# Optimization experiments

Measured on AMD Instinct MI355X. Metric: run time of the kernel, lower is better.

## Reference

```python
import jax, jax.numpy as jnp
import numpy as np

FILTER_LENGTH = 1024
HOP_LENGTH = 512
CUTOFF = FILTER_LENGTH // 2 + 1  # 513


def _make_forward_basis():
    n = FILTER_LENGTH
    fb = np.fft.fft(np.eye(n))
    fb = np.vstack([np.real(fb[:CUTOFF, :]), np.imag(fb[:CUTOFF, :])]).astype(np.float32)  # [2*cutoff, n]
    # hann window, fftbins=True (periodic); win_length == filter_length so pad_center is a no-op
    win = (0.5 - 0.5 * np.cos(2.0 * np.pi * np.arange(n) / n)).astype(np.float32)
    return jnp.asarray(fb * win[None, :])


def setup_inputs() -> dict:
    key = jax.random.key(0)
    B, T = 8, 1048576
    input_data = jax.random.normal(key, (B, T), dtype=jnp.float32)
    return {
        "input_data": input_data,
        "forward_basis": _make_forward_basis(),  # [1026, 1024]
        "eps": jnp.float32(1e-9),
    }


def reference(input_data, forward_basis, eps):
    pad = FILTER_LENGTH // 2
    x = jnp.pad(input_data, ((0, 0), (pad, pad)), mode="reflect")  # [B, T + filter_length]
    n_frames = (x.shape[1] - FILTER_LENGTH) // HOP_LENGTH + 1
    # gather overlapping frames: [B, n_frames, filter_length]
    idx = jnp.arange(n_frames)[:, None] * HOP_LENGTH + jnp.arange(FILTER_LENGTH)[None, :]
    frames = x[:, idx]
    # DFT via dense matmul: [B, 2*cutoff, n_frames]
    ft = jnp.einsum("fk,bnk->bfn", forward_basis, frames)
    real, imag = ft[:, :CUTOFF, :], ft[:, CUTOFF:, :]
    return jnp.sqrt(real * real + imag * imag + eps)
```

## Files before the change

kernel.cpp:

```cpp
#include <hip/hip_runtime.h>

#define T_LEN   1048576
#define NPAD    1049600
#define NFRAMES 2049
#define BATCH   8
#define NJ      (BATCH * NFRAMES)
#define NSEG    2050
#define CUT     513
#define MROWS   1026
#define MPAD    1152
#define OUT_BF  (CUT * NFRAMES)

typedef __attribute__((ext_vector_type(8))) short bf16x8_t;
typedef __attribute__((ext_vector_type(4))) float f32x4_t;

static __device__ __forceinline__ ushort f2bf(float f) {
    union { float f; unsigned u; } a;
    a.f = f;
    unsigned r = a.u + 0x7fffu + ((a.u >> 16) & 1u);
    return (ushort)(r >> 16);
}

static __device__ __forceinline__ void gl_lds16(const ushort* g, ushort* s) {
    __builtin_amdgcn_global_load_lds(
        (__attribute__((address_space(1))) void*)g,
        (__attribute__((address_space(3))) void*)s,
        16, 0, 0);
}

__global__ void pad_kernel(const float* __restrict__ in, ushort* __restrict__ xpad) {
    int g  = blockIdx.x * 256 + threadIdx.x;
    int b  = g / (NPAD / 8);
    int c  = g - b * (NPAD / 8);
    int i0 = c * 8;
    const float* inb = in + (size_t)b * T_LEN;
    ushort o[8];
    if (i0 >= 512 && i0 + 7 < 512 + T_LEN) {
        const float4 v0 = *(const float4*)(inb + (i0 - 512));
        const float4 v1 = *(const float4*)(inb + (i0 - 512) + 4);
        o[0]=f2bf(v0.x); o[1]=f2bf(v0.y); o[2]=f2bf(v0.z); o[3]=f2bf(v0.w);
        o[4]=f2bf(v1.x); o[5]=f2bf(v1.y); o[6]=f2bf(v1.z); o[7]=f2bf(v1.w);
    } else {
        for (int t = 0; t < 8; ++t) {
            int i = i0 + t;
            int src = (i < 512) ? (512 - i)
                    : (i < 512 + T_LEN) ? (i - 512)
                    : (2 * T_LEN + 510 - i);
            o[t] = f2bf(inb[src]);
        }
    }
    *(ulonglong2*)(xpad + (size_t)b * NPAD + i0) = *(ulonglong2*)o;
}

__global__ void basis_kernel(const float* __restrict__ fb, ushort* __restrict__ A2) {
    int g  = blockIdx.x * 256 + threadIdx.x;
    int r  = g >> 8;
    int cq = (g & 255) * 4;
    ushort4 o;
    if (r < MROWS) {
        int f = r >> 1, h = r & 1;
        const float4 v = *(const float4*)(fb + (size_t)(f + h * CUT) * 1024 + cq);
        o = make_ushort4(f2bf(v.x), f2bf(v.y), f2bf(v.z), f2bf(v.w));
    } else {
        o = make_ushort4(0, 0, 0, 0);
    }
    *(ushort4*)(A2 + (size_t)r * 1024 + cq) = o;
}

__global__ __launch_bounds__(256) void gemm_kernel(
        const ushort* __restrict__ A2, const ushort* __restrict__ xpad,
        float* __restrict__ out, const float* __restrict__ epsp) {
    __shared__ __align__(16) ushort ldsA0[128 * 64];
    __shared__ __align__(16) ushort ldsA1[128 * 64];
    __shared__ __align__(16) ushort ldsB [136 * 64];

    const int tid  = threadIdx.x;
    const int wave = tid >> 6, lane = tid & 63;
    const int quad = lane >> 4, l15 = lane & 15;
    const int m0 = blockIdx.x * 128;
    const int j0 = blockIdx.y * 128;
    const int wm = (wave >> 1) * 64;
    const int wj = (wave & 1) * 64;

    const int sr  = lane >> 3;
    const int sc8 = ((lane & 7) ^ sr) * 8;

    const int b0 = j0 / NFRAMES;
    const int S0 = j0 + b0;

    int aoff[4], boff[4], boffx = 0;
    for (int t = 0; t < 4; ++t) {
        const int r = (wave * 4 + t) * 8 + sr;
        aoff[t] = (m0 + r) * 1024 + sc8;
        int S = S0 + r; if (S > BATCH * NSEG - 1) S = BATCH * NSEG - 1;
        int bb = S / NSEG, ss = S - bb * NSEG;
        boff[t] = bb * NPAD + ss * 512 + sc8;
    }
    {
        int S = S0 + 128 + sr; if (S > BATCH * NSEG - 1) S = BATCH * NSEG - 1;
        int bb = S / NSEG, ss = S - bb * NSEG;
        boffx = bb * NPAD + ss * 512 + sc8;
    }

    int rowb[4];
    for (int jx = 0; jx < 4; ++jx) {
        const int j = j0 + wj + jx * 16 + l15;
        rowb[jx] = wj + jx * 16 + l15 + (j / NFRAMES - b0);
    }

    f32x4_t acc[4][4] = {};

    for (int kt = 0; kt < 8; ++kt) {
        const int k0 = kt * 64;
        __syncthreads();
        for (int t = 0; t < 4; ++t) {
            gl_lds16(A2 + aoff[t] + k0,        &ldsA0[(wave * 4 + t) * 512]);
            gl_lds16(A2 + aoff[t] + 512 + k0,  &ldsA1[(wave * 4 + t) * 512]);
            gl_lds16(xpad + boff[t] + k0,      &ldsB [(wave * 4 + t) * 512]);
        }
        if (wave == 0) gl_lds16(xpad + boffx + k0, &ldsB[16 * 512]);
        __syncthreads();
        for (int kk = 0; kk < 2; ++kk) {
            const int cb = kk * 4 + quad;
            bf16x8_t a0[4], a1[4], bf0[4], bf1[4];
            const int asw = (cb ^ (l15 & 7)) * 8;
            for (int i = 0; i < 4; ++i) {
                const int ro = (wm + i * 16 + l15) * 64;
                a0[i] = *(const bf16x8_t*)&ldsA0[ro + asw];
                a1[i] = *(const bf16x8_t*)&ldsA1[ro + asw];
            }
            for (int jx = 0; jx < 4; ++jx) {
                const int r0 = rowb[jx];
                const int r1 = r0 + 1;
                bf0[jx] = *(const bf16x8_t*)&ldsB[r0 * 64 + ((cb ^ (r0 & 7)) * 8)];
                bf1[jx] = *(const bf16x8_t*)&ldsB[r1 * 64 + ((cb ^ (r1 & 7)) * 8)];
            }
            for (int i = 0; i < 4; ++i)
                for (int jx = 0; jx < 4; ++jx) {
                    acc[i][jx] = __builtin_amdgcn_mfma_f32_16x16x32_bf16(
                        a0[i], bf0[jx], acc[i][jx], 0, 0, 0);
                    acc[i][jx] = __builtin_amdgcn_mfma_f32_16x16x32_bf16(
                        a1[i], bf1[jx], acc[i][jx], 0, 0, 0);
                }
        }
    }

    const float eps = *epsp;
    for (int tj = 0; tj < 4; ++tj) {
        const int j = j0 + wj + tj * 16 + l15;
        if (j >= NJ) continue;
        const int b = j / NFRAMES;
        const int n = j - b * NFRAMES;
        float* ob = out + (size_t)b * OUT_BF + n;
        for (int ti = 0; ti < 4; ++ti) {
            const int M  = m0 + wm + ti * 16 + quad * 4;
            const int f0 = M >> 1;
            f32x4_t a = acc[ti][tj];
            if (f0 < CUT)
                ob[(size_t)f0 * NFRAMES] = sqrtf(a.x * a.x + a.y * a.y + eps);
            if (f0 + 1 < CUT)
                ob[(size_t)(f0 + 1) * NFRAMES] = sqrtf(a.z * a.z + a.w * a.w + eps);
        }
    }
}

extern "C" void kernel_launch(void* const* d_in, const int* in_sizes, int n_in,
                              void* d_out, int out_size, void* d_ws, size_t ws_size,
                              hipStream_t stream) {
    const float* in   = (const float*)d_in[0];
    const float* fb   = (const float*)d_in[1];
    const float* epsp = (const float*)d_in[2];
    float* out = (float*)d_out;

    ushort* A2   = (ushort*)d_ws;
    ushort* xpad = (ushort*)((char*)d_ws + (size_t)MPAD * 1024 * 2);

    pad_kernel<<<dim3(BATCH * (NPAD / 8) / 256), dim3(256), 0, stream>>>(in, xpad);
    basis_kernel<<<dim3(MPAD), dim3(256), 0, stream>>>(fb, A2);
    gemm_kernel<<<dim3(MPAD / 128, (NJ + 127) / 128), dim3(256), 0, stream>>>(A2, xpad, out, epsp);
}
```

Baseline: 134.8 us.

## Halve GEMM k-tile LDS footprint, raise occupancy, and remap blocks for L2 locality

The GEMM k-step drops from 64 to 32 with a new swizzled LDS layout, which halves shared memory per block so more blocks fit per CU. Launch bounds now request 5 blocks per SM. The 2D grid becomes a 1D grid remapped so groups of 8 frame tiles share the 9 basis tiles, aiming at better L2 reuse. LDS read addresses are precomputed into registers. The trade-off is twice as many barrier and load rounds per tile and some idle blocks that exit early.

```diff
diff --git a/kernel.cpp b/kernel.cpp
--- a/kernel.cpp
+++ b/kernel.cpp
@@ -6,10 +6,12 @@
 #define BATCH   8
 #define NJ      (BATCH * NFRAMES)
 #define NSEG    2050
+#define SMAX    (BATCH * NSEG - 1)
 #define CUT     513
 #define MROWS   1026
 #define MPAD    1152
 #define OUT_BF  (CUT * NFRAMES)
+#define NJT     129
 
 typedef __attribute__((ext_vector_type(8))) short bf16x8_t;
 typedef __attribute__((ext_vector_type(4))) float f32x4_t;
@@ -67,82 +69,107 @@
     *(ushort4*)(A2 + (size_t)r * 1024 + cq) = o;
 }
 
-__global__ __launch_bounds__(256) void gemm_kernel(
+__global__ __launch_bounds__(256, 5) void gemm_kernel(
         const ushort* __restrict__ A2, const ushort* __restrict__ xpad,
         float* __restrict__ out, const float* __restrict__ epsp) {
-    __shared__ __align__(16) ushort ldsA0[128 * 64];
-    __shared__ __align__(16) ushort ldsA1[128 * 64];
-    __shared__ __align__(16) ushort ldsB [136 * 64];
+    __shared__ __align__(16) ushort ldsA0[64 * 64];
+    __shared__ __align__(16) ushort ldsA1[64 * 64];
+    __shared__ __align__(16) ushort ldsB [72 * 64];
+
+    const int bid = blockIdx.x;
+    const int jt  = (bid / 72) * 8 + (bid & 7);
+    const int mt  = (bid >> 3) % 9;
+    if (jt >= NJT) return;
 
     const int tid  = threadIdx.x;
     const int wave = tid >> 6, lane = tid & 63;
     const int quad = lane >> 4, l15 = lane & 15;
-    const int m0 = blockIdx.x * 128;
-    const int j0 = blockIdx.y * 128;
+    const int m0 = mt * 128;
+    const int j0 = jt * 128;
     const int wm = (wave >> 1) * 64;
     const int wj = (wave & 1) * 64;
 
-    const int sr  = lane >> 3;
-    const int sc8 = ((lane & 7) ^ sr) * 8;
-
     const int b0 = j0 / NFRAMES;
     const int S0 = j0 + b0;
 
-    int aoff[4], boff[4], boffx = 0;
-    for (int t = 0; t < 4; ++t) {
-        const int r = (wave * 4 + t) * 8 + sr;
-        aoff[t] = (m0 + r) * 1024 + sc8;
-        int S = S0 + r; if (S > BATCH * NSEG - 1) S = BATCH * NSEG - 1;
+    const int li   = lane >> 3;
+    const int lc   = (lane & 7) ^ li;
+    const int half = lc >> 2;
+    const int kch8 = (lc & 3) * 8;
+
+    int aoff[2];
+    for (int t = 0; t < 2; ++t) {
+        const int q = wave * 2 + t;
+        const int arow = (8 * q + li) + 64 * half;
+        aoff[t] = (m0 + arow) * 1024 + kch8;
+    }
+    int boff[2], boffx = 0;
+    for (int t = 0; t < 2; ++t) {
+        const int q = wave * 2 + t;
+        int S = S0 + (8 * q + li) + 72 * half; if (S > SMAX) S = SMAX;
         int bb = S / NSEG, ss = S - bb * NSEG;
-        boff[t] = bb * NPAD + ss * 512 + sc8;
+        boff[t] = bb * NPAD + ss * 512 + kch8;
     }
     {
-        int S = S0 + 128 + sr; if (S > BATCH * NSEG - 1) S = BATCH * NSEG - 1;
+        int S = S0 + (64 + li) + 72 * half; if (S > SMAX) S = SMAX;
         int bb = S / NSEG, ss = S - bb * NSEG;
-        boffx = bb * NPAD + ss * 512 + sc8;
-    }
-
-    int rowb[4];
+        boffx = bb * NPAD + ss * 512 + kch8;
+    }
+
+    int addrA[4], addrB0[4], addrB1[4];
+    for (int i = 0; i < 4; ++i) {
+        const int m  = wm + i * 16 + l15;
+        const int lr = m & 63;
+        const int p  = (((m >> 6) << 2) + quad) ^ (lr & 7);
+        addrA[i] = lr * 64 + p * 8;
+    }
     for (int jx = 0; jx < 4; ++jx) {
-        const int j = j0 + wj + jx * 16 + l15;
-        rowb[jx] = wj + jx * 16 + l15 + (j / NFRAMES - b0);
+        const int j  = j0 + wj + jx * 16 + l15;
+        const int r0 = wj + jx * 16 + l15 + (j / NFRAMES - b0);
+        const int r1 = r0 + 1;
+        const int lr0 = (r0 >= 72) ? r0 - 72 : r0;
+        const int lr1 = (r1 >= 72) ? r1 - 72 : r1;
+        const int p0  = (((r0 >= 72) ? 4 : 0) + quad) ^ (lr0 & 7);
+        const int p1  = (((r1 >= 72) ? 4 : 0) + quad) ^ (lr1 & 7);
+        addrB0[jx] = lr0 * 64 + p0 * 8;
+        addrB1[jx] = lr1 * 64 + p1 * 8;
     }
 
     f32x4_t acc[4][4] = {};
 
-    for (int kt = 0; kt < 8; ++kt) {
-        const int k0 = kt * 64;
+    for (int kt = 0; kt < 16; ++kt) {
+        const int k32 = kt * 32;
         __syncthreads();
-        for (int t = 0; t < 4; ++t) {
-            gl_lds16(A2 + aoff[t] + k0,        &ldsA0[(wave * 4 + t) * 512]);
-            gl_lds16(A2 + aoff[t] + 512 + k0,  &ldsA1[(wave * 4 + t) * 512]);
-            gl_lds16(xpad + boff[t] + k0,      &ldsB [(wave * 4 + t) * 512]);
-        }
-        if (wave == 0) gl_lds16(xpad + boffx + k0, &ldsB[16 * 512]);
+        #pragma unroll
+        for (int t = 0; t < 2; ++t) {
+            const int q = wave * 2 + t;
+            gl_lds16(A2 + aoff[t] + k32,        &ldsA0[q * 512]);
+            gl_lds16(A2 + aoff[t] + 512 + k32,  &ldsA1[q * 512]);
+            gl_lds16(xpad + boff[t] + k32,      &ldsB [q * 512]);
+        }
+        if (wave == 0) gl_lds16(xpad + boffx + k32, &ldsB[8 * 512]);
         __syncthreads();
-        for (int kk = 0; kk < 2; ++kk) {
-            const int cb = kk * 4 + quad;
-            bf16x8_t a0[4], a1[4], bf0[4], bf1[4];
-            const int asw = (cb ^ (l15 & 7)) * 8;
-            for (int i = 0; i < 4; ++i) {
-                const int ro = (wm + i * 16 + l15) * 64;
-                a0[i] = *(const bf16x8_t*)&ldsA0[ro + asw];
-                a1[i] = *(const bf16x8_t*)&ldsA1[ro + asw];
+
+        bf16x8_t a0[4], a1[4], bf0[4], bf1[4];
+        #pragma unroll
+        for (int i = 0; i < 4; ++i) {
+            a0[i] = *(const bf16x8_t*)&ldsA0[addrA[i]];
+            a1[i] = *(const bf16x8_t*)&ldsA1[addrA[i]];
+        }
+        #pragma unroll
+        for (int jx = 0; jx < 4; ++jx) {
+            bf0[jx] = *(const bf16x8_t*)&ldsB[addrB0[jx]];
+            bf1[jx] = *(const bf16x8_t*)&ldsB[addrB1[jx]];
+        }
+        #pragma unroll
+        for (int i = 0; i < 4; ++i)
+            #pragma unroll
+            for (int jx = 0; jx < 4; ++jx) {
+                acc[i][jx] = __builtin_amdgcn_mfma_f32_16x16x32_bf16(
+                    a0[i], bf0[jx], acc[i][jx], 0, 0, 0);
+                acc[i][jx] = __builtin_amdgcn_mfma_f32_16x16x32_bf16(
+                    a1[i], bf1[jx], acc[i][jx], 0, 0, 0);
             }
-            for (int jx = 0; jx < 4; ++jx) {
-                const int r0 = rowb[jx];
-                const int r1 = r0 + 1;
-                bf0[jx] = *(const bf16x8_t*)&ldsB[r0 * 64 + ((cb ^ (r0 & 7)) * 8)];
-                bf1[jx] = *(const bf16x8_t*)&ldsB[r1 * 64 + ((cb ^ (r1 & 7)) * 8)];
-            }
-            for (int i = 0; i < 4; ++i)
-                for (int jx = 0; jx < 4; ++jx) {
-                    acc[i][jx] = __builtin_amdgcn_mfma_f32_16x16x32_bf16(
-                        a0[i], bf0[jx], acc[i][jx], 0, 0, 0);
-                    acc[i][jx] = __builtin_amdgcn_mfma_f32_16x16x32_bf16(
-                        a1[i], bf1[jx], acc[i][jx], 0, 0, 0);
-                }
-        }
     }
 
     const float eps = *epsp;
@@ -177,5 +204,5 @@
 
     pad_kernel<<<dim3(BATCH * (NPAD / 8) / 256), dim3(256), 0, stream>>>(in, xpad);
     basis_kernel<<<dim3(MPAD), dim3(256), 0, stream>>>(fb, A2);
-    gemm_kernel<<<dim3(MPAD / 128, (NJ + 127) / 128), dim3(256), 0, stream>>>(A2, xpad, out, epsp);
-}
+    gemm_kernel<<<dim3(17 * 72), dim3(256), 0, stream>>>(A2, xpad, out, epsp);
+}
```

Result: slower. 146.6 us (+8.8%).

## Double-buffer B tiles in LDS, load A from global, fuse prep kernels, swizzle grid

Applied to the files above, without the earlier changes.

Merges the pad and basis conversion kernels into one launch. In the GEMM, the A (basis) operand is now read directly from global memory into registers instead of staged through LDS, and the B (frames) tile is double-buffered with a prefetch of the next k-slice before computing the current one, removing one barrier per iteration. The grid becomes 1D with a grouped mapping of 8 j-tiles across 9 m-tiles for L2 reuse, and launch_bounds asks for 3 blocks per CU. The risk is that uncoalesced global A loads add latency and register pressure.

```diff
diff --git a/kernel.cpp b/kernel.cpp
--- a/kernel.cpp
+++ b/kernel.cpp
@@ -6,10 +6,13 @@
 #define BATCH   8
 #define NJ      (BATCH * NFRAMES)
 #define NSEG    2050
+#define SMAX    (BATCH * NSEG - 1)
 #define CUT     513
 #define MROWS   1026
 #define MPAD    1152
 #define OUT_BF  (CUT * NFRAMES)
+#define NJT     129
+#define PAD_BLOCKS (BATCH * (NPAD / 8) / 256)
 
 typedef __attribute__((ext_vector_type(8))) short bf16x8_t;
 typedef __attribute__((ext_vector_type(4))) float f32x4_t;
@@ -28,114 +31,132 @@
         16, 0, 0);
 }
 
-__global__ void pad_kernel(const float* __restrict__ in, ushort* __restrict__ xpad) {
-    int g  = blockIdx.x * 256 + threadIdx.x;
-    int b  = g / (NPAD / 8);
-    int c  = g - b * (NPAD / 8);
-    int i0 = c * 8;
-    const float* inb = in + (size_t)b * T_LEN;
-    ushort o[8];
-    if (i0 >= 512 && i0 + 7 < 512 + T_LEN) {
-        const float4 v0 = *(const float4*)(inb + (i0 - 512));
-        const float4 v1 = *(const float4*)(inb + (i0 - 512) + 4);
-        o[0]=f2bf(v0.x); o[1]=f2bf(v0.y); o[2]=f2bf(v0.z); o[3]=f2bf(v0.w);
-        o[4]=f2bf(v1.x); o[5]=f2bf(v1.y); o[6]=f2bf(v1.z); o[7]=f2bf(v1.w);
+__global__ void prep_kernel(const float* __restrict__ in, const float* __restrict__ fb,
+                            ushort* __restrict__ xpad, ushort* __restrict__ A2) {
+    const int tid = threadIdx.x;
+    if (blockIdx.x < PAD_BLOCKS) {
+        int g  = blockIdx.x * 256 + tid;
+        int b  = g / (NPAD / 8);
+        int c  = g - b * (NPAD / 8);
+        int i0 = c * 8;
+        const float* inb = in + (size_t)b * T_LEN;
+        ushort o[8];
+        if (i0 >= 512 && i0 + 7 < 512 + T_LEN) {
+            const float4 v0 = *(const float4*)(inb + (i0 - 512));
+            const float4 v1 = *(const float4*)(inb + (i0 - 512) + 4);
+            o[0]=f2bf(v0.x); o[1]=f2bf(v0.y); o[2]=f2bf(v0.z); o[3]=f2bf(v0.w);
+            o[4]=f2bf(v1.x); o[5]=f2bf(v1.y); o[6]=f2bf(v1.z); o[7]=f2bf(v1.w);
+        } else {
+            for (int t = 0; t < 8; ++t) {
+                int i = i0 + t;
+                int src = (i < 512) ? (512 - i)
+                        : (i < 512 + T_LEN) ? (i - 512)
+                        : (2 * T_LEN + 510 - i);
+                o[t] = f2bf(inb[src]);
+            }
+        }
+        *(ulonglong2*)(xpad + (size_t)b * NPAD + i0) = *(ulonglong2*)o;
     } else {
-        for (int t = 0; t < 8; ++t) {
-            int i = i0 + t;
-            int src = (i < 512) ? (512 - i)
-                    : (i < 512 + T_LEN) ? (i - 512)
-                    : (2 * T_LEN + 510 - i);
-            o[t] = f2bf(inb[src]);
-        }
-    }
-    *(ulonglong2*)(xpad + (size_t)b * NPAD + i0) = *(ulonglong2*)o;
-}
-
-__global__ void basis_kernel(const float* __restrict__ fb, ushort* __restrict__ A2) {
-    int g  = blockIdx.x * 256 + threadIdx.x;
-    int r  = g >> 8;
-    int cq = (g & 255) * 4;
-    ushort4 o;
-    if (r < MROWS) {
-        int f = r >> 1, h = r & 1;
-        const float4 v = *(const float4*)(fb + (size_t)(f + h * CUT) * 1024 + cq);
-        o = make_ushort4(f2bf(v.x), f2bf(v.y), f2bf(v.z), f2bf(v.w));
-    } else {
-        o = make_ushort4(0, 0, 0, 0);
-    }
-    *(ushort4*)(A2 + (size_t)r * 1024 + cq) = o;
-}
-
-__global__ __launch_bounds__(256) void gemm_kernel(
+        int g  = (blockIdx.x - PAD_BLOCKS) * 256 + tid;
+        int r  = g >> 8;
+        int cq = (g & 255) * 4;
+        ushort4 o;
+        if (r < MROWS) {
+            int f = r >> 1, h = r & 1;
+            const float4 v = *(const float4*)(fb + (size_t)(f + h * CUT) * 1024 + cq);
+            o = make_ushort4(f2bf(v.x), f2bf(v.y), f2bf(v.z), f2bf(v.w));
+        } else {
+            o = make_ushort4(0, 0, 0, 0);
+        }
+        *(ushort4*)(A2 + (size_t)r * 1024 + cq) = o;
+    }
+}
+
+__global__ __launch_bounds__(256, 3) void gemm_kernel(
         const ushort* __restrict__ A2, const ushort* __restrict__ xpad,
         float* __restrict__ out, const float* __restrict__ epsp) {
-    __shared__ __align__(16) ushort ldsA0[128 * 64];
-    __shared__ __align__(16) ushort ldsA1[128 * 64];
-    __shared__ __align__(16) ushort ldsB [136 * 64];
+    __shared__ __align__(16) ushort ldsB[2][136 * 64];
+
+    const int bid = blockIdx.x;
+    const int jt  = (bid / 72) * 8 + (bid & 7);
+    const int mt  = (bid >> 3) % 9;
+    if (jt >= NJT) return;
 
     const int tid  = threadIdx.x;
     const int wave = tid >> 6, lane = tid & 63;
     const int quad = lane >> 4, l15 = lane & 15;
-    const int m0 = blockIdx.x * 128;
-    const int j0 = blockIdx.y * 128;
-    const int wm = (wave >> 1) * 64;
-    const int wj = (wave & 1) * 64;
+    const int m0 = mt * 128, j0 = jt * 128;
+    const int wm = (wave >> 1) * 64, wj = (wave & 1) * 64;
+    const int b0 = j0 / NFRAMES;
+    const int S0 = j0 + b0;
 
     const int sr  = lane >> 3;
     const int sc8 = ((lane & 7) ^ sr) * 8;
-
-    const int b0 = j0 / NFRAMES;
-    const int S0 = j0 + b0;
-
-    int aoff[4], boff[4], boffx = 0;
+    int boff[4], boffx;
     for (int t = 0; t < 4; ++t) {
-        const int r = (wave * 4 + t) * 8 + sr;
-        aoff[t] = (m0 + r) * 1024 + sc8;
-        int S = S0 + r; if (S > BATCH * NSEG - 1) S = BATCH * NSEG - 1;
+        int S = S0 + (wave * 4 + t) * 8 + sr; if (S > SMAX) S = SMAX;
         int bb = S / NSEG, ss = S - bb * NSEG;
         boff[t] = bb * NPAD + ss * 512 + sc8;
     }
     {
-        int S = S0 + 128 + sr; if (S > BATCH * NSEG - 1) S = BATCH * NSEG - 1;
+        int S = S0 + 128 + sr; if (S > SMAX) S = SMAX;
         int bb = S / NSEG, ss = S - bb * NSEG;
         boffx = bb * NPAD + ss * 512 + sc8;
     }
 
-    int rowb[4];
+    int r0base[4], r1base[4], r0s[4], r1s[4];
     for (int jx = 0; jx < 4; ++jx) {
-        const int j = j0 + wj + jx * 16 + l15;
-        rowb[jx] = wj + jx * 16 + l15 + (j / NFRAMES - b0);
-    }
+        const int j  = j0 + wj + jx * 16 + l15;
+        const int r0 = wj + jx * 16 + l15 + (j / NFRAMES - b0);
+        const int r1 = r0 + 1;
+        r0base[jx] = r0 * 64;  r0s[jx] = r0 & 7;
+        r1base[jx] = r1 * 64;  r1s[jx] = r1 & 7;
+    }
+
+    const ushort* arow[4];
+    for (int i = 0; i < 4; ++i)
+        arow[i] = A2 + (size_t)(m0 + wm + i * 16 + l15) * 1024 + quad * 8;
 
     f32x4_t acc[4][4] = {};
 
+    {
+        ushort* buf = &ldsB[0][0];
+        #pragma unroll
+        for (int t = 0; t < 4; ++t)
+            gl_lds16(xpad + boff[t], buf + (wave * 4 + t) * 512);
+        if (wave == 0) gl_lds16(xpad + boffx, buf + 16 * 512);
+    }
+
     for (int kt = 0; kt < 8; ++kt) {
-        const int k0 = kt * 64;
         __syncthreads();
-        for (int t = 0; t < 4; ++t) {
-            gl_lds16(A2 + aoff[t] + k0,        &ldsA0[(wave * 4 + t) * 512]);
-            gl_lds16(A2 + aoff[t] + 512 + k0,  &ldsA1[(wave * 4 + t) * 512]);
-            gl_lds16(xpad + boff[t] + k0,      &ldsB [(wave * 4 + t) * 512]);
-        }
-        if (wave == 0) gl_lds16(xpad + boffx + k0, &ldsB[16 * 512]);
-        __syncthreads();
+        if (kt < 7) {
+            ushort* buf = &ldsB[(kt + 1) & 1][0];
+            const int ko = (kt + 1) * 64;
+            #pragma unroll
+            for (int t = 0; t < 4; ++t)
+                gl_lds16(xpad + boff[t] + ko, buf + (wave * 4 + t) * 512);
+            if (wave == 0) gl_lds16(xpad + boffx + ko, buf + 16 * 512);
+        }
+        const ushort* bb_ = &ldsB[kt & 1][0];
+
+        #pragma unroll
         for (int kk = 0; kk < 2; ++kk) {
             const int cb = kk * 4 + quad;
+            const int ko = kt * 64 + kk * 32;
             bf16x8_t a0[4], a1[4], bf0[4], bf1[4];
-            const int asw = (cb ^ (l15 & 7)) * 8;
+            #pragma unroll
             for (int i = 0; i < 4; ++i) {
-                const int ro = (wm + i * 16 + l15) * 64;
-                a0[i] = *(const bf16x8_t*)&ldsA0[ro + asw];
-                a1[i] = *(const bf16x8_t*)&ldsA1[ro + asw];
+                a0[i] = *(const bf16x8_t*)(arow[i] + ko);
+                a1[i] = *(const bf16x8_t*)(arow[i] + 512 + ko);
             }
+            #pragma unroll
             for (int jx = 0; jx < 4; ++jx) {
-                const int r0 = rowb[jx];
-                const int r1 = r0 + 1;
-                bf0[jx] = *(const bf16x8_t*)&ldsB[r0 * 64 + ((cb ^ (r0 & 7)) * 8)];
-                bf1[jx] = *(const bf16x8_t*)&ldsB[r1 * 64 + ((cb ^ (r1 & 7)) * 8)];
+                bf0[jx] = *(const bf16x8_t*)&bb_[r0base[jx] + ((cb ^ r0s[jx]) * 8)];
+                bf1[jx] = *(const bf16x8_t*)&bb_[r1base[jx] + ((cb ^ r1s[jx]) * 8)];
             }
+            #pragma unroll
             for (int i = 0; i < 4; ++i)
+                #pragma unroll
                 for (int jx = 0; jx < 4; ++jx) {
                     acc[i][jx] = __builtin_amdgcn_mfma_f32_16x16x32_bf16(
                         a0[i], bf0[jx], acc[i][jx], 0, 0, 0);
@@ -175,7 +196,6 @@
     ushort* A2   = (ushort*)d_ws;
     ushort* xpad = (ushort*)((char*)d_ws + (size_t)MPAD * 1024 * 2);
 
-    pad_kernel<<<dim3(BATCH * (NPAD / 8) / 256), dim3(256), 0, stream>>>(in, xpad);
-    basis_kernel<<<dim3(MPAD), dim3(256), 0, stream>>>(fb, A2);
-    gemm_kernel<<<dim3(MPAD / 128, (NJ + 127) / 128), dim3(256), 0, stream>>>(A2, xpad, out, epsp);
-}
+    prep_kernel<<<dim3(PAD_BLOCKS + MPAD), dim3(256), 0, stream>>>(in, fb, xpad, A2);
+    gemm_kernel<<<dim3(17 * 72), dim3(256), 0, stream>>>(A2, xpad, out, epsp);
+}
```

Result: slower. 191.4 us (+42.1%).
